# Performance work log

Hardware: AMD Instinct MI355X
Metric: run time of the kernel (lower is better)

The kernel has to match this reference:

```python
import jax, jax.numpy as jnp
import numpy as np

B, L, C, H, OUT = 32, 2048, 1024, 16, 128
HID = 256  # mlp hidden fixed in source


def setup_inputs() -> dict:
    key = jax.random.key(0)
    ks = jax.random.split(key, 12)
    w = lambda i, shape: jax.random.normal(ks[i], shape, dtype=jnp.float32) * 0.02
    return {
        "fvec_c": jax.random.normal(ks[0], (B, 1, C), dtype=jnp.float32),
        "fvec_seq": jax.random.normal(ks[1], (B, L, C), dtype=jnp.float32),
        "dis_enc_c": jax.random.normal(ks[2], (1, B, C), dtype=jnp.float32),
        "dis_enc_seq": jax.random.normal(ks[3], (1, B, L, C), dtype=jnp.float32),
        "in_proj_w": w(4, (3 * C, C)),
        "in_proj_b": jnp.zeros((3 * C,), jnp.float32),
        "out_w": w(5, (C, C)),
        "out_b": jnp.zeros((C,), jnp.float32),
        "ln1_g": jnp.ones((C,), jnp.float32),
        "ln1_b": jnp.zeros((C,), jnp.float32),
        "w1": w(6, (HID, C)),
        "b1": jnp.zeros((HID,), jnp.float32),
        "ln2_g": jnp.ones((HID,), jnp.float32),
        "ln2_b": jnp.zeros((HID,), jnp.float32),
        "w2": w(7, (OUT, HID)),
        "b2": jnp.zeros((OUT,), jnp.float32),
    }


def _ln(x, g, b, eps=1e-5):
    m = x.mean(-1, keepdims=True)
    v = ((x - m) ** 2).mean(-1, keepdims=True)
    return (x - m) * jax.lax.rsqrt(v + eps) * g + b


def reference(fvec_c, fvec_seq, dis_enc_c, dis_enc_seq, in_proj_w, in_proj_b,
              out_w, out_b, ln1_g, ln1_b, w1, b1, ln2_g, ln2_b, w2, b2):
    b, l, embed_dim = fvec_seq.shape
    hd = embed_dim // H
    scale = float(hd) ** -0.5
    wq, wk, wv = in_proj_w[:embed_dim], in_proj_w[embed_dim:2 * embed_dim], in_proj_w[2 * embed_dim:]
    bq, bk, bv = in_proj_b[:embed_dim], in_proj_b[embed_dim:2 * embed_dim], in_proj_b[2 * embed_dim:]

    q = (fvec_c @ wq.T + bq) * scale                 # [B,1,C]
    k = fvec_seq @ wk.T + bk                         # [B,L,C]
    v = fvec_seq @ wv.T + bv                         # [B,L,C]
    q_r = (dis_enc_c[0] @ wq.T + bq) * scale         # [B,C]
    k_r = dis_enc_seq[0] @ wk.T + bk                 # [B,L,C]

    qh = q.reshape(b, 1, H, hd)
    kh = k.reshape(b, l, H, hd)
    vh = v.reshape(b, l, H, hd)
    qrh = q_r.reshape(b, 1, H, hd)
    krh = k_r.reshape(b, l, H, hd)

    # disentangled scores: content-content + content-pos + pos-content -> [B,H,1,L]
    attn = (jnp.einsum('bnhc,bmhc->bhnm', qh, kh)
            + jnp.einsum('bnhc,bvhc->bhnv', qh, krh)
            + jnp.einsum('bmhc,bvhc->bhmv', qrh, kh))
    a = jax.nn.softmax(attn, axis=-1)                # [B,H,1,L]

    v_o = jnp.einsum('bhnl,blhc->bnhc', a, vh).reshape(b, 1, embed_dim)
    v_o = v_o @ out_w.T + out_b                      # [B,1,C]

    # mlp head (dropout is identity at inference)
    x = _ln(v_o, ln1_g, ln1_b)
    x = _ln(x @ w1.T + b1, ln2_g, ln2_b)
    return x @ w2.T + b2                             # [B,1,OUT]
```

## Files before the change

kernel.cpp:

```cpp
#include <hip/hip_runtime.h>
#include <hip/hip_bf16.h>
#include <cstdint>
#include <cstddef>

#define B_   32
#define L_   2048
#define C_   1024
#define H_   16
#define HD_  64
#define HID_ 256
#define OUT_ 128
#define NS_  8
#define RPB_ (L_/NS_)
#define RPI_ 4
#define ITERS_ (RPB_/RPI_)

#define WS_U1   0
#define WS_U2   (WS_U1 + B_*C_)
#define WS_A1   (WS_U2 + B_*C_)
#define WS_A2   (WS_A1 + B_*H_*C_)
#define WS_CST  (WS_A2 + B_*H_*C_)
#define WS_MP   (WS_CST + B_*H_)
#define WS_ZP   (WS_MP + B_*NS_*H_)
#define WS_SP   (WS_ZP + B_*NS_*H_)
#define WS_SFIN (WS_SP + B_*NS_*H_*C_)
#define WS_VO   (WS_SFIN + B_*H_*C_)
#define WS_O    (WS_VO + B_*C_)

template <int CTRL>
__device__ __forceinline__ float dpp_add(float x) {
  int t = __builtin_amdgcn_update_dpp(0, __float_as_int(x), CTRL, 0xF, 0xF, true);
  return x + __int_as_float(t);
}
__device__ __forceinline__ float wave_sum_bcast(float x) {
  x = dpp_add<0x111>(x);
  x = dpp_add<0x112>(x);
  x = dpp_add<0x114>(x);
  x = dpp_add<0x118>(x);
  x = dpp_add<0x142>(x);
  x = dpp_add<0x143>(x);
  return __int_as_float(__builtin_amdgcn_readlane(__float_as_int(x), 63));
}

__global__ __launch_bounds__(256) void prep_q(
    const float* __restrict__ fvec_c, const float* __restrict__ dis_enc_c,
    const float* __restrict__ in_proj_w, const float* __restrict__ in_proj_b,
    float* __restrict__ ws) {
  int tid = blockIdx.x * 256 + threadIdx.x;
  int b = tid & (B_ - 1);
  int i = tid >> 5;
  const float* x = fvec_c + b * C_;
  const float* d = dis_enc_c + b * C_;
  const float* w = in_proj_w + (size_t)i * C_;
  float ax = 0.f, ad = 0.f;
  for (int k = 0; k < C_; k += 4) {
    float4 wv = *(const float4*)(w + k);
    float4 xv = *(const float4*)(x + k);
    float4 dv = *(const float4*)(d + k);
    ax += wv.x*xv.x + wv.y*xv.y + wv.z*xv.z + wv.w*xv.w;
    ad += wv.x*dv.x + wv.y*dv.y + wv.z*dv.z + wv.w*dv.w;
  }
  float q  = (ax + in_proj_b[i]) * 0.125f;
  float qr = (ad + in_proj_b[i]) * 0.125f;
  ws[WS_U1 + b*C_ + i] = q + qr;
  ws[WS_U2 + b*C_ + i] = q;
}

__global__ __launch_bounds__(256) void prep_A(
    const float* __restrict__ Wk, const float* __restrict__ bk,
    float* __restrict__ ws) {
  int b = blockIdx.x, h = blockIdx.y, t = threadIdx.x;
  __shared__ float su1[HD_], su2[HD_];
  if (t < HD_) {
    su1[t] = ws[WS_U1 + b*C_ + h*HD_ + t];
    su2[t] = ws[WS_U2 + b*C_ + h*HD_ + t];
  }
  __syncthreads();
  if (t == 0) {
    float cs = 0.f;
    for (int j = 0; j < HD_; ++j) cs += (su1[j] + su2[j]) * bk[h*HD_ + j];
    ws[WS_CST + b*H_ + h] = cs;
  }
  for (int jj = 0; jj < 4; ++jj) {
    int c = t + 256 * jj;
    float a1 = 0.f, a2 = 0.f;
    #pragma unroll
    for (int j = 0; j < HD_; ++j) {
      float w = Wk[(size_t)(h*HD_ + j) * C_ + c];
      a1 += su1[j] * w;
      a2 += su2[j] * w;
    }
    ws[WS_A1 + (size_t)(b*H_ + h)*C_ + c] = a1;
    ws[WS_A2 + (size_t)(b*H_ + h)*C_ + c] = a2;
  }
}

__global__ __launch_bounds__(512, 1) void flash(
    const float* __restrict__ fvec_seq, const float* __restrict__ dis_enc_seq,
    float* __restrict__ ws) {
  int b = blockIdx.x, s = blockIdx.y;
  int t = threadIdx.x;
  int wv_ = t >> 6, ln = t & 63;
  int h0 = 2 * wv_, h1 = 2 * wv_ + 1;

  __shared__ float bx[2][RPI_][C_];
  __shared__ float bd[2][RPI_][C_];

  float A10[16], A11[16], A20[16], A21[16];
  {
    const float* a10 = ws + WS_A1 + (size_t)(b*H_ + h0)*C_;
    const float* a11 = ws + WS_A1 + (size_t)(b*H_ + h1)*C_;
    const float* a20 = ws + WS_A2 + (size_t)(b*H_ + h0)*C_;
    const float* a21 = ws + WS_A2 + (size_t)(b*H_ + h1)*C_;
    #pragma unroll
    for (int j = 0; j < 4; ++j) {
      int c = 4*ln + 256*j;
      *(float4*)&A10[4*j] = *(const float4*)(a10 + c);
      *(float4*)&A11[4*j] = *(const float4*)(a11 + c);
      *(float4*)&A20[4*j] = *(const float4*)(a20 + c);
      *(float4*)&A21[4*j] = *(const float4*)(a21 + c);
    }
  }
  float c0 = ws[WS_CST + b*H_ + h0];
  float c1 = ws[WS_CST + b*H_ + h1];

  float S0[16], S1[16];
  #pragma unroll
  for (int i = 0; i < 16; ++i) { S0[i] = 0.f; S1[i] = 0.f; }
  float m0 = -1e30f, m1 = -1e30f, Z0 = 0.f, Z1 = 0.f;

  const int l0 = s * RPB_;
  const float* xbase = fvec_seq    + ((size_t)b * L_ + l0) * C_;
  const float* dbase = dis_enc_seq + ((size_t)b * L_ + l0) * C_;

  #pragma unroll
  for (int k = 0; k < 4; ++k) {
    int idx = t + 512 * k;
    int which = idx >> 10;
    int r = (idx >> 8) & 3;
    int off = (idx & 255) * 4;
    float4 v = *(const float4*)((which ? dbase : xbase) + r * C_ + off);
    if (which) *(float4*)&bd[0][r][off] = v; else *(float4*)&bx[0][r][off] = v;
  }
  __syncthreads();

  for (int it = 0; it < ITERS_; ++it) {
    int cur = it & 1, nxt = cur ^ 1;
    float4 st[4];
    bool have = (it + 1 < ITERS_);
    if (have) {
      const float* xb = xbase + (size_t)(it + 1) * RPI_ * C_;
      const float* db = dbase + (size_t)(it + 1) * RPI_ * C_;
      #pragma unroll
      for (int k = 0; k < 4; ++k) {
        int idx = t + 512 * k;
        int which = idx >> 10;
        int r = (idx >> 8) & 3;
        int off = (idx & 255) * 4;
        st[k] = *(const float4*)((which ? db : xb) + r * C_ + off);
      }
    }
    #pragma unroll
    for (int rr = 0; rr < RPI_; ++rr) {
      float4 xv[4], dv[4];
      #pragma unroll
      for (int j = 0; j < 4; ++j) {
        xv[j] = *(const float4*)&bx[cur][rr][4*ln + 256*j];
        dv[j] = *(const float4*)&bd[cur][rr][4*ln + 256*j];
      }
      float p0 = 0.f, p1 = 0.f;
      #pragma unroll
      for (int j = 0; j < 4; ++j) {
        const float* x4 = (const float*)&xv[j];
        const float* d4 = (const float*)&dv[j];
        #pragma unroll
        for (int i = 0; i < 4; ++i) {
          p0 += A10[4*j+i]*x4[i] + A20[4*j+i]*d4[i];
          p1 += A11[4*j+i]*x4[i] + A21[4*j+i]*d4[i];
        }
      }
      p0 = wave_sum_bcast(p0) + c0;
      p1 = wave_sum_bcast(p1) + c1;
      if (p0 > m0) {
        float fs = __expf(m0 - p0);
        Z0 *= fs;
        #pragma unroll
        for (int i = 0; i < 16; ++i) S0[i] *= fs;
        m0 = p0;
      }
      {
        float e = __expf(p0 - m0);
        Z0 += e;
        #pragma unroll
        for (int j = 0; j < 4; ++j) {
          const float* x4 = (const float*)&xv[j];
          #pragma unroll
          for (int i = 0; i < 4; ++i) S0[4*j+i] += e * x4[i];
        }
      }
      if (p1 > m1) {
        float fs = __expf(m1 - p1);
        Z1 *= fs;
        #pragma unroll
        for (int i = 0; i < 16; ++i) S1[i] *= fs;
        m1 = p1;
      }
      {
        float e = __expf(p1 - m1);
        Z1 += e;
        #pragma unroll
        for (int j = 0; j < 4; ++j) {
          const float* x4 = (const float*)&xv[j];
          #pragma unroll
          for (int i = 0; i < 4; ++i) S1[4*j+i] += e * x4[i];
        }
      }
    }
    if (have) {
      #pragma unroll
      for (int k = 0; k < 4; ++k) {
        int idx = t + 512 * k;
        int which = idx >> 10;
        int r = (idx >> 8) & 3;
        int off = (idx & 255) * 4;
        if (which) *(float4*)&bd[nxt][r][off] = st[k]; else *(float4*)&bx[nxt][r][off] = st[k];
      }
    }
    __syncthreads();
  }

  {
    float* sp0 = ws + WS_SP + ((size_t)(b*NS_ + s)*H_ + h0) * C_;
    float* sp1 = ws + WS_SP + ((size_t)(b*NS_ + s)*H_ + h1) * C_;
    #pragma unroll
    for (int j = 0; j < 4; ++j) {
      *(float4*)(sp0 + 4*ln + 256*j) = *(float4*)&S0[4*j];
      *(float4*)(sp1 + 4*ln + 256*j) = *(float4*)&S1[4*j];
    }
    if (ln == 0) {
      ws[WS_MP + (b*NS_ + s)*H_ + h0] = m0;
      ws[WS_MP + (b*NS_ + s)*H_ + h1] = m1;
      ws[WS_ZP + (b*NS_ + s)*H_ + h0] = Z0;
      ws[WS_ZP + (b*NS_ + s)*H_ + h1] = Z1;
    }
  }
}

__global__ __launch_bounds__(256) void reduce_s(float* __restrict__ ws) {
  int b = blockIdx.x, h = blockIdx.y, t = threadIdx.x;
  float ms[NS_], wsc[NS_];
  float m = -1e30f;
  #pragma unroll
  for (int s = 0; s < NS_; ++s) {
    ms[s] = ws[WS_MP + (b*NS_ + s)*H_ + h];
    m = fmaxf(m, ms[s]);
  }
  float Z = 0.f;
  #pragma unroll
  for (int s = 0; s < NS_; ++s) {
    wsc[s] = __expf(ms[s] - m);
    Z += ws[WS_ZP + (b*NS_ + s)*H_ + h] * wsc[s];
  }
  float inv = 1.0f / Z;
  for (int jj = 0; jj < 4; ++jj) {
    int c = t + 256 * jj;
    float acc = 0.f;
    #pragma unroll
    for (int s = 0; s < NS_; ++s)
      acc += ws[WS_SP + ((size_t)(b*NS_ + s)*H_ + h)*C_ + c] * wsc[s];
    ws[WS_SFIN + (size_t)(b*H_ + h)*C_ + c] = acc * inv;
  }
}

__global__ __launch_bounds__(256) void vo_proj(
    const float* __restrict__ in_proj_w, const float* __restrict__ in_proj_b,
    float* __restrict__ ws) {
  int tid = blockIdx.x * 256 + threadIdx.x;
  int b = tid & (B_ - 1);
  int i = tid >> 5;
  const float* w = in_proj_w + (size_t)(2*C_ + i) * C_;
  const float* sf = ws + WS_SFIN + (size_t)(b*H_ + (i >> 6)) * C_;
  float acc = in_proj_b[2*C_ + i];
  for (int k = 0; k < C_; k += 4) {
    float4 a = *(const float4*)(w + k);
    float4 x = *(const float4*)(sf + k);
    acc += a.x*x.x + a.y*x.y + a.z*x.z + a.w*x.w;
  }
  ws[WS_VO + b*C_ + i] = acc;
}

__global__ __launch_bounds__(256) void out_proj(
    const float* __restrict__ out_w, const float* __restrict__ out_b,
    float* __restrict__ ws) {
  int tid = blockIdx.x * 256 + threadIdx.x;
  int b = tid & (B_ - 1);
  int j = tid >> 5;
  const float* w = out_w + (size_t)j * C_;
  const float* x = ws + WS_VO + b*C_;
  float acc = out_b[j];
  for (int k = 0; k < C_; k += 4) {
    float4 a = *(const float4*)(w + k);
    float4 v = *(const float4*)(x + k);
    acc += a.x*v.x + a.y*v.y + a.z*v.z + a.w*v.w;
  }
  ws[WS_O + b*C_ + j] = acc;
}

__global__ __launch_bounds__(256) void mlp_tail(
    const float* __restrict__ ln1_g, const float* __restrict__ ln1_b,
    const float* __restrict__ w1, const float* __restrict__ b1,
    const float* __restrict__ ln2_g, const float* __restrict__ ln2_b,
    const float* __restrict__ w2, const float* __restrict__ b2,
    const float* __restrict__ ws, float* __restrict__ out) {
  int b = blockIdx.x, t = threadIdx.x;
  __shared__ float xr[C_];
  __shared__ float xh[HID_];
  __shared__ float red[8];
  const float* o = ws + WS_O + b*C_;
  float v[4];
  float s = 0.f, sq = 0.f;
  #pragma unroll
  for (int j = 0; j < 4; ++j) {
    v[j] = o[t + 256*j];
    s += v[j];
    sq += v[j]*v[j];
  }
  s = wave_sum_bcast(s); sq = wave_sum_bcast(sq);
  int w = t >> 6;
  if ((t & 63) == 0) { red[w] = s; red[4+w] = sq; }
  __syncthreads();
  s  = red[0]+red[1]+red[2]+red[3];
  sq = red[4]+red[5]+red[6]+red[7];
  float mean = s * (1.f/1024.f);
  float var  = sq * (1.f/1024.f) - mean*mean;
  float rs = rsqrtf(var + 1e-5f);
  #pragma unroll
  for (int j = 0; j < 4; ++j) {
    int c = t + 256*j;
    xr[c] = (v[j] - mean) * rs * ln1_g[c] + ln1_b[c];
  }
  __syncthreads();
  float acc = b1[t];
  const float* wr = w1 + (size_t)t * C_;
  for (int k = 0; k < C_; k += 4) {
    float4 a = *(const float4*)(wr + k);
    acc += a.x*xr[k] + a.y*xr[k+1] + a.z*xr[k+2] + a.w*xr[k+3];
  }
  float s2 = wave_sum_bcast(acc), sq2 = wave_sum_bcast(acc*acc);
  if ((t & 63) == 0) { red[w] = s2; red[4+w] = sq2; }
  __syncthreads();
  s2  = red[0]+red[1]+red[2]+red[3];
  sq2 = red[4]+red[5]+red[6]+red[7];
  float m2 = s2 * (1.f/256.f);
  float v2 = sq2 * (1.f/256.f) - m2*m2;
  float rs2 = rsqrtf(v2 + 1e-5f);
  xh[t] = (acc - m2) * rs2 * ln2_g[t] + ln2_b[t];
  __syncthreads();
  if (t < OUT_) {
    float a2 = b2[t];
    const float* wr2 = w2 + (size_t)t * HID_;
    for (int k = 0; k < HID_; k += 4) {
      float4 a = *(const float4*)(wr2 + k);
      a2 += a.x*xh[k] + a.y*xh[k+1] + a.z*xh[k+2] + a.w*xh[k+3];
    }
    out[b*OUT_ + t] = a2;
  }
}

extern "C" void kernel_launch(void* const* d_in, const int* in_sizes, int n_in,
                              void* d_out, int out_size, void* d_ws, size_t ws_size,
                              hipStream_t stream) {
  (void)in_sizes; (void)n_in; (void)out_size; (void)ws_size;
  const float* fvec_c      = (const float*)d_in[0];
  const float* fvec_seq    = (const float*)d_in[1];
  const float* dis_enc_c   = (const float*)d_in[2];
  const float* dis_enc_seq = (const float*)d_in[3];
  const float* in_proj_w   = (const float*)d_in[4];
  const float* in_proj_b   = (const float*)d_in[5];
  const float* out_w       = (const float*)d_in[6];
  const float* out_b       = (const float*)d_in[7];
  const float* ln1_g       = (const float*)d_in[8];
  const float* ln1_b       = (const float*)d_in[9];
  const float* w1          = (const float*)d_in[10];
  const float* b1          = (const float*)d_in[11];
  const float* ln2_g       = (const float*)d_in[12];
  const float* ln2_b       = (const float*)d_in[13];
  const float* w2          = (const float*)d_in[14];
  const float* b2          = (const float*)d_in[15];
  float* ws  = (float*)d_ws;
  float* out = (float*)d_out;

  prep_q  <<<dim3((B_*C_)/256), 256, 0, stream>>>(fvec_c, dis_enc_c, in_proj_w, in_proj_b, ws);
  prep_A  <<<dim3(B_, H_),      256, 0, stream>>>(in_proj_w + (size_t)C_*C_, in_proj_b + C_, ws);
  flash   <<<dim3(B_, NS_),     512, 0, stream>>>(fvec_seq, dis_enc_seq, ws);
  reduce_s<<<dim3(B_, H_),      256, 0, stream>>>(ws);
  vo_proj <<<dim3((B_*C_)/256), 256, 0, stream>>>(in_proj_w, in_proj_b, ws);
  out_proj<<<dim3((B_*C_)/256), 256, 0, stream>>>(out_w, out_b, ws);
  mlp_tail<<<dim3(B_),          256, 0, stream>>>(ln1_g, ln1_b, w1, b1, ln2_g, ln2_b, w2, b2, ws, out);
}
```

Measured before the change: 1.042 ms.

## Split disentangled attention into positional and content passes; use wave-per-output GEMVs

The single streaming-softmax flash kernel is replaced by two kernels. The first computes the positional score term from dis_enc_seq into a workspace buffer. The second streams fvec_seq, adds that stored term to the content score, and accumulates exp-weighted sums. Both use 1024-thread blocks, twice as many sequence splits, and global_load_lds double buffering. The running max is dropped, so exp is applied to raw scores, which can overflow for large score magnitudes. The projection and MLP kernels are remapped from one thread per output with serial 1024-long loops to one wave per output with DPP reductions, to raise parallelism in these latency-bound GEMVs.

```diff
diff --git a/kernel.cpp b/kernel.cpp
--- a/kernel.cpp
+++ b/kernel.cpp
@@ -10,18 +10,16 @@
 #define HD_  64
 #define HID_ 256
 #define OUT_ 128
-#define NS_  8
+#define NS_  16
 #define RPB_ (L_/NS_)
-#define RPI_ 4
-#define ITERS_ (RPB_/RPI_)
 
 #define WS_U1   0
 #define WS_U2   (WS_U1 + B_*C_)
 #define WS_A1   (WS_U2 + B_*C_)
 #define WS_A2   (WS_A1 + B_*H_*C_)
 #define WS_CST  (WS_A2 + B_*H_*C_)
-#define WS_MP   (WS_CST + B_*H_)
-#define WS_ZP   (WS_MP + B_*NS_*H_)
+#define WS_G    (WS_CST + B_*H_)
+#define WS_ZP   (WS_G + B_*L_*H_)
 #define WS_SP   (WS_ZP + B_*NS_*H_)
 #define WS_SFIN (WS_SP + B_*NS_*H_*C_)
 #define WS_VO   (WS_SFIN + B_*H_*C_)
@@ -41,29 +39,38 @@
   x = dpp_add<0x143>(x);
   return __int_as_float(__builtin_amdgcn_readlane(__float_as_int(x), 63));
 }
-
-__global__ __launch_bounds__(256) void prep_q(
+__device__ __forceinline__ float red8(float x) {
+  x = dpp_add<0x114>(x);
+  x = dpp_add<0x112>(x);
+  x = dpp_add<0x111>(x);
+  return x;
+}
+
+__global__ __launch_bounds__(512) void prep_q(
     const float* __restrict__ fvec_c, const float* __restrict__ dis_enc_c,
     const float* __restrict__ in_proj_w, const float* __restrict__ in_proj_b,
     float* __restrict__ ws) {
-  int tid = blockIdx.x * 256 + threadIdx.x;
-  int b = tid & (B_ - 1);
-  int i = tid >> 5;
-  const float* x = fvec_c + b * C_;
-  const float* d = dis_enc_c + b * C_;
-  const float* w = in_proj_w + (size_t)i * C_;
+  int t = threadIdx.x, wv = t >> 6, ln = t & 63;
+  int task = blockIdx.x * 8 + wv;
+  int i = task >> 5, b = task & 31;
+  const float4* wr = (const float4*)(in_proj_w + (size_t)i * C_) + ln * 4;
+  const float4* xp = (const float4*)(fvec_c + b * C_) + ln * 4;
+  const float4* dp = (const float4*)(dis_enc_c + b * C_) + ln * 4;
   float ax = 0.f, ad = 0.f;
-  for (int k = 0; k < C_; k += 4) {
-    float4 wv = *(const float4*)(w + k);
-    float4 xv = *(const float4*)(x + k);
-    float4 dv = *(const float4*)(d + k);
-    ax += wv.x*xv.x + wv.y*xv.y + wv.z*xv.z + wv.w*xv.w;
-    ad += wv.x*dv.x + wv.y*dv.y + wv.z*dv.z + wv.w*dv.w;
-  }
-  float q  = (ax + in_proj_b[i]) * 0.125f;
-  float qr = (ad + in_proj_b[i]) * 0.125f;
-  ws[WS_U1 + b*C_ + i] = q + qr;
-  ws[WS_U2 + b*C_ + i] = q;
+  #pragma unroll
+  for (int k = 0; k < 4; ++k) {
+    float4 w = wr[k], x = xp[k], d = dp[k];
+    ax += w.x*x.x + w.y*x.y + w.z*x.z + w.w*x.w;
+    ad += w.x*d.x + w.y*d.y + w.z*d.z + w.w*d.w;
+  }
+  ax = wave_sum_bcast(ax); ad = wave_sum_bcast(ad);
+  if (ln == 0) {
+    float bq = in_proj_b[i];
+    float q  = (ax + bq) * 0.125f;
+    float qr = (ad + bq) * 0.125f;
+    ws[WS_U1 + b*C_ + i] = q + qr;
+    ws[WS_U2 + b*C_ + i] = q;
+  }
 }
 
 __global__ __launch_bounds__(256) void prep_A(
@@ -95,275 +102,276 @@
   }
 }
 
-__global__ __launch_bounds__(512, 1) void flash(
-    const float* __restrict__ fvec_seq, const float* __restrict__ dis_enc_seq,
-    float* __restrict__ ws) {
-  int b = blockIdx.x, s = blockIdx.y;
-  int t = threadIdx.x;
-  int wv_ = t >> 6, ln = t & 63;
-  int h0 = 2 * wv_, h1 = 2 * wv_ + 1;
-
-  __shared__ float bx[2][RPI_][C_];
-  __shared__ float bd[2][RPI_][C_];
-
-  float A10[16], A11[16], A20[16], A21[16];
+__global__ __launch_bounds__(1024, 4) void pass_d(
+    const float* __restrict__ dis_enc_seq, float* __restrict__ ws) {
+  int b = blockIdx.x, spl = blockIdx.y;
+  int t = threadIdx.x, wv = t >> 6, ln = t & 63;
+  int s = ln >> 3, sub = ln & 7;
+  int h0 = 2*s, h1 = 2*s + 1;
+  int cb = wv*64 + sub*8;
+
+  __shared__ float bd[2][4][C_];
+  __shared__ float part[4][16][16];
+
+  float A2a[8], A2b[8];
   {
-    const float* a10 = ws + WS_A1 + (size_t)(b*H_ + h0)*C_;
-    const float* a11 = ws + WS_A1 + (size_t)(b*H_ + h1)*C_;
-    const float* a20 = ws + WS_A2 + (size_t)(b*H_ + h0)*C_;
-    const float* a21 = ws + WS_A2 + (size_t)(b*H_ + h1)*C_;
-    #pragma unroll
-    for (int j = 0; j < 4; ++j) {
-      int c = 4*ln + 256*j;
-      *(float4*)&A10[4*j] = *(const float4*)(a10 + c);
-      *(float4*)&A11[4*j] = *(const float4*)(a11 + c);
-      *(float4*)&A20[4*j] = *(const float4*)(a20 + c);
-      *(float4*)&A21[4*j] = *(const float4*)(a21 + c);
-    }
-  }
-  float c0 = ws[WS_CST + b*H_ + h0];
-  float c1 = ws[WS_CST + b*H_ + h1];
-
-  float S0[16], S1[16];
-  #pragma unroll
-  for (int i = 0; i < 16; ++i) { S0[i] = 0.f; S1[i] = 0.f; }
-  float m0 = -1e30f, m1 = -1e30f, Z0 = 0.f, Z1 = 0.f;
-
-  const int l0 = s * RPB_;
-  const float* xbase = fvec_seq    + ((size_t)b * L_ + l0) * C_;
-  const float* dbase = dis_enc_seq + ((size_t)b * L_ + l0) * C_;
-
-  #pragma unroll
-  for (int k = 0; k < 4; ++k) {
-    int idx = t + 512 * k;
-    int which = idx >> 10;
-    int r = (idx >> 8) & 3;
-    int off = (idx & 255) * 4;
-    float4 v = *(const float4*)((which ? dbase : xbase) + r * C_ + off);
-    if (which) *(float4*)&bd[0][r][off] = v; else *(float4*)&bx[0][r][off] = v;
-  }
-  __syncthreads();
-
-  for (int it = 0; it < ITERS_; ++it) {
-    int cur = it & 1, nxt = cur ^ 1;
-    float4 st[4];
-    bool have = (it + 1 < ITERS_);
-    if (have) {
-      const float* xb = xbase + (size_t)(it + 1) * RPI_ * C_;
-      const float* db = dbase + (size_t)(it + 1) * RPI_ * C_;
-      #pragma unroll
-      for (int k = 0; k < 4; ++k) {
-        int idx = t + 512 * k;
-        int which = idx >> 10;
-        int r = (idx >> 8) & 3;
-        int off = (idx & 255) * 4;
-        st[k] = *(const float4*)((which ? db : xb) + r * C_ + off);
-      }
-    }
-    #pragma unroll
-    for (int rr = 0; rr < RPI_; ++rr) {
-      float4 xv[4], dv[4];
-      #pragma unroll
-      for (int j = 0; j < 4; ++j) {
-        xv[j] = *(const float4*)&bx[cur][rr][4*ln + 256*j];
-        dv[j] = *(const float4*)&bd[cur][rr][4*ln + 256*j];
-      }
+    const float* pa = ws + WS_A2 + (size_t)(b*H_ + h0)*C_ + cb;
+    const float* pb = ws + WS_A2 + (size_t)(b*H_ + h1)*C_ + cb;
+    *(float4*)&A2a[0] = *(const float4*)pa; *(float4*)&A2a[4] = *(const float4*)(pa+4);
+    *(float4*)&A2b[0] = *(const float4*)pb; *(float4*)&A2b[4] = *(const float4*)(pb+4);
+  }
+  float csth = ws[WS_CST + b*H_ + (ln & 15)];
+  const float* dbase = dis_enc_seq + ((size_t)b*L_ + spl*RPB_)*C_;
+  float* gdst = ws + WS_G + ((size_t)b*L_ + spl*RPB_)*H_;
+
+  {
+    int r = wv >> 2, seg = wv & 3;
+    float* dst = &bd[0][r][seg*256];
+    const float* src = dbase + (size_t)r*C_ + seg*256 + ln*4;
+    __builtin_amdgcn_global_load_lds(src, dst, 16, 0, 0);
+  }
+  __syncthreads();
+
+  for (int g = 0; g < RPB_/4; ++g) {
+    int cur = g & 1;
+    if (g + 1 < RPB_/4) {
+      int r = wv >> 2, seg = wv & 3;
+      float* dst = &bd[cur^1][r][seg*256];
+      const float* src = dbase + (size_t)((g+1)*4 + r)*C_ + seg*256 + ln*4;
+      __builtin_amdgcn_global_load_lds(src, dst, 16, 0, 0);
+    }
+    #pragma unroll
+    for (int r = 0; r < 4; ++r) {
+      float dv[8];
+      *(float4*)&dv[0] = *(const float4*)&bd[cur][r][cb];
+      *(float4*)&dv[4] = *(const float4*)&bd[cur][r][cb+4];
       float p0 = 0.f, p1 = 0.f;
       #pragma unroll
-      for (int j = 0; j < 4; ++j) {
-        const float* x4 = (const float*)&xv[j];
-        const float* d4 = (const float*)&dv[j];
-        #pragma unroll
-        for (int i = 0; i < 4; ++i) {
-          p0 += A10[4*j+i]*x4[i] + A20[4*j+i]*d4[i];
-          p1 += A11[4*j+i]*x4[i] + A21[4*j+i]*d4[i];
-        }
+      for (int j = 0; j < 8; ++j) { p0 += A2a[j]*dv[j]; p1 += A2b[j]*dv[j]; }
+      p0 = red8(p0); p1 = red8(p1);
+      if (sub == 7) *(float2*)&part[r][wv][2*s] = make_float2(p0, p1);
+    }
+    __syncthreads();
+    if (wv == 0) {
+      int h = ln & 15, r = ln >> 4;
+      float ps = 0.f;
+      #pragma unroll
+      for (int w2 = 0; w2 < 16; ++w2) ps += part[r][w2][h];
+      gdst[(size_t)(g*4 + r)*H_ + h] = ps + csth;
+    }
+    __syncthreads();
+  }
+}
+
+__global__ __launch_bounds__(1024, 4) void flash_x(
+    const float* __restrict__ fvec_seq, float* __restrict__ ws) {
+  int b = blockIdx.x, spl = blockIdx.y;
+  int t = threadIdx.x, wv = t >> 6, ln = t & 63;
+  int s = ln >> 3, sub = ln & 7;
+  int h0 = 2*s, h1 = 2*s + 1;
+  int cb = wv*64 + sub*8;
+
+  __shared__ float bx[2][2][C_];
+  __shared__ float part[2][16][16];
+  __shared__ float ebuf[2][16];
+  __shared__ float zred[2][16];
+
+  float A1a[8], A1b[8];
+  {
+    const float* pa = ws + WS_A1 + (size_t)(b*H_ + h0)*C_ + cb;
+    const float* pb = ws + WS_A1 + (size_t)(b*H_ + h1)*C_ + cb;
+    *(float4*)&A1a[0] = *(const float4*)pa; *(float4*)&A1a[4] = *(const float4*)(pa+4);
+    *(float4*)&A1b[0] = *(const float4*)pb; *(float4*)&A1b[4] = *(const float4*)(pb+4);
+  }
+  float S0[8], S1[8];
+  #pragma unroll
+  for (int j = 0; j < 8; ++j) { S0[j] = 0.f; S1[j] = 0.f; }
+  float zacc = 0.f;
+
+  const float* xbase = fvec_seq + ((size_t)b*L_ + spl*RPB_)*C_;
+  const float* gsrc  = ws + WS_G + ((size_t)b*L_ + spl*RPB_)*H_;
+
+  if (wv < 8) {
+    int r = wv >> 2, seg = wv & 3;
+    float* dst = &bx[0][r][seg*256];
+    const float* src = xbase + (size_t)r*C_ + seg*256 + ln*4;
+    __builtin_amdgcn_global_load_lds(src, dst, 16, 0, 0);
+  }
+  __syncthreads();
+
+  for (int g = 0; g < RPB_/2; ++g) {
+    int cur = g & 1;
+    if (g + 1 < RPB_/2) {
+      if (wv < 8) {
+        int r = wv >> 2, seg = wv & 3;
+        float* dst = &bx[cur^1][r][seg*256];
+        const float* src = xbase + (size_t)((g+1)*2 + r)*C_ + seg*256 + ln*4;
+        __builtin_amdgcn_global_load_lds(src, dst, 16, 0, 0);
       }
-      p0 = wave_sum_bcast(p0) + c0;
-      p1 = wave_sum_bcast(p1) + c1;
-      if (p0 > m0) {
-        float fs = __expf(m0 - p0);
-        Z0 *= fs;
-        #pragma unroll
-        for (int i = 0; i < 16; ++i) S0[i] *= fs;
-        m0 = p0;
-      }
-      {
-        float e = __expf(p0 - m0);
-        Z0 += e;
-        #pragma unroll
-        for (int j = 0; j < 4; ++j) {
-          const float* x4 = (const float*)&xv[j];
-          #pragma unroll
-          for (int i = 0; i < 4; ++i) S0[4*j+i] += e * x4[i];
-        }
-      }
-      if (p1 > m1) {
-        float fs = __expf(m1 - p1);
-        Z1 *= fs;
-        #pragma unroll
-        for (int i = 0; i < 16; ++i) S1[i] *= fs;
-        m1 = p1;
-      }
-      {
-        float e = __expf(p1 - m1);
-        Z1 += e;
-        #pragma unroll
-        for (int j = 0; j < 4; ++j) {
-          const float* x4 = (const float*)&xv[j];
-          #pragma unroll
-          for (int i = 0; i < 4; ++i) S1[4*j+i] += e * x4[i];
-        }
-      }
-    }
-    if (have) {
+    }
+    float x0[8], x1[8];
+    *(float4*)&x0[0] = *(const float4*)&bx[cur][0][cb];
+    *(float4*)&x0[4] = *(const float4*)&bx[cur][0][cb+4];
+    *(float4*)&x1[0] = *(const float4*)&bx[cur][1][cb];
+    *(float4*)&x1[4] = *(const float4*)&bx[cur][1][cb+4];
+    float p00 = 0.f, p01 = 0.f, p10 = 0.f, p11 = 0.f;
+    #pragma unroll
+    for (int j = 0; j < 8; ++j) {
+      p00 += A1a[j]*x0[j]; p01 += A1b[j]*x0[j];
+      p10 += A1a[j]*x1[j]; p11 += A1b[j]*x1[j];
+    }
+    p00 = red8(p00); p01 = red8(p01); p10 = red8(p10); p11 = red8(p11);
+    if (sub == 7) {
+      *(float2*)&part[0][wv][2*s] = make_float2(p00, p01);
+      *(float2*)&part[1][wv][2*s] = make_float2(p10, p11);
+    }
+    __syncthreads();
+    if (wv == 0 && ln < 32) {
+      int h = ln & 15, r = ln >> 4;
+      float ps = 0.f;
       #pragma unroll
-      for (int k = 0; k < 4; ++k) {
-        int idx = t + 512 * k;
-        int which = idx >> 10;
-        int r = (idx >> 8) & 3;
-        int off = (idx & 255) * 4;
-        if (which) *(float4*)&bd[nxt][r][off] = st[k]; else *(float4*)&bx[nxt][r][off] = st[k];
-      }
+      for (int w2 = 0; w2 < 16; ++w2) ps += part[r][w2][h];
+      float e = __expf(ps + gsrc[(size_t)(g*2 + r)*H_ + h]);
+      zacc += e;
+      ebuf[r][h] = e;
     }
     __syncthreads();
-  }
-
+    float2 e0 = *(const float2*)&ebuf[0][2*s];
+    float2 e1 = *(const float2*)&ebuf[1][2*s];
+    #pragma unroll
+    for (int j = 0; j < 8; ++j) {
+      S0[j] += e0.x*x0[j] + e1.x*x1[j];
+      S1[j] += e0.y*x0[j] + e1.y*x1[j];
+    }
+  }
   {
-    float* sp0 = ws + WS_SP + ((size_t)(b*NS_ + s)*H_ + h0) * C_;
-    float* sp1 = ws + WS_SP + ((size_t)(b*NS_ + s)*H_ + h1) * C_;
-    #pragma unroll
-    for (int j = 0; j < 4; ++j) {
-      *(float4*)(sp0 + 4*ln + 256*j) = *(float4*)&S0[4*j];
-      *(float4*)(sp1 + 4*ln + 256*j) = *(float4*)&S1[4*j];
-    }
-    if (ln == 0) {
-      ws[WS_MP + (b*NS_ + s)*H_ + h0] = m0;
-      ws[WS_MP + (b*NS_ + s)*H_ + h1] = m1;
-      ws[WS_ZP + (b*NS_ + s)*H_ + h0] = Z0;
-      ws[WS_ZP + (b*NS_ + s)*H_ + h1] = Z1;
-    }
-  }
+    float* sp0 = ws + WS_SP + ((size_t)((b*NS_ + spl)*H_ + h0))*C_ + cb;
+    float* sp1 = ws + WS_SP + ((size_t)((b*NS_ + spl)*H_ + h1))*C_ + cb;
+    #pragma unroll
+    for (int j = 0; j < 8; ++j) { sp0[j] = S0[j]; sp1[j] = S1[j]; }
+  }
+  __syncthreads();
+  if (wv == 0 && ln < 32) zred[ln >> 4][ln & 15] = zacc;
+  __syncthreads();
+  if (t < 16) ws[WS_ZP + (b*NS_ + spl)*H_ + t] = zred[0][t] + zred[1][t];
 }
 
 __global__ __launch_bounds__(256) void reduce_s(float* __restrict__ ws) {
   int b = blockIdx.x, h = blockIdx.y, t = threadIdx.x;
-  float ms[NS_], wsc[NS_];
-  float m = -1e30f;
-  #pragma unroll
-  for (int s = 0; s < NS_; ++s) {
-    ms[s] = ws[WS_MP + (b*NS_ + s)*H_ + h];
-    m = fmaxf(m, ms[s]);
-  }
   float Z = 0.f;
   #pragma unroll
-  for (int s = 0; s < NS_; ++s) {
-    wsc[s] = __expf(ms[s] - m);
-    Z += ws[WS_ZP + (b*NS_ + s)*H_ + h] * wsc[s];
-  }
+  for (int sp = 0; sp < NS_; ++sp) Z += ws[WS_ZP + (b*NS_ + sp)*H_ + h];
   float inv = 1.0f / Z;
+  #pragma unroll
   for (int jj = 0; jj < 4; ++jj) {
     int c = t + 256 * jj;
     float acc = 0.f;
     #pragma unroll
-    for (int s = 0; s < NS_; ++s)
-      acc += ws[WS_SP + ((size_t)(b*NS_ + s)*H_ + h)*C_ + c] * wsc[s];
+    for (int sp = 0; sp < NS_; ++sp)
+      acc += ws[WS_SP + ((size_t)((b*NS_ + sp)*H_ + h))*C_ + c];
     ws[WS_SFIN + (size_t)(b*H_ + h)*C_ + c] = acc * inv;
   }
 }
 
-__global__ __launch_bounds__(256) void vo_proj(
+__global__ __launch_bounds__(512) void vo_proj(
     const float* __restrict__ in_proj_w, const float* __restrict__ in_proj_b,
     float* __restrict__ ws) {
-  int tid = blockIdx.x * 256 + threadIdx.x;
-  int b = tid & (B_ - 1);
-  int i = tid >> 5;
-  const float* w = in_proj_w + (size_t)(2*C_ + i) * C_;
-  const float* sf = ws + WS_SFIN + (size_t)(b*H_ + (i >> 6)) * C_;
-  float acc = in_proj_b[2*C_ + i];
-  for (int k = 0; k < C_; k += 4) {
-    float4 a = *(const float4*)(w + k);
-    float4 x = *(const float4*)(sf + k);
+  int t = threadIdx.x, wv = t >> 6, ln = t & 63;
+  int task = blockIdx.x * 8 + wv;
+  int i = task >> 5, b = task & 31;
+  const float4* wr = (const float4*)(in_proj_w + (size_t)(2*C_ + i)*C_) + ln * 4;
+  const float4* sf = (const float4*)(ws + WS_SFIN + (size_t)(b*H_ + (i >> 6))*C_) + ln * 4;
+  float acc = 0.f;
+  #pragma unroll
+  for (int k = 0; k < 4; ++k) {
+    float4 a = wr[k], x = sf[k];
     acc += a.x*x.x + a.y*x.y + a.z*x.z + a.w*x.w;
   }
-  ws[WS_VO + b*C_ + i] = acc;
-}
-
-__global__ __launch_bounds__(256) void out_proj(
+  acc = wave_sum_bcast(acc);
+  if (ln == 0) ws[WS_VO + b*C_ + i] = acc + in_proj_b[2*C_ + i];
+}
+
+__global__ __launch_bounds__(512) void out_proj(
     const float* __restrict__ out_w, const float* __restrict__ out_b,
     float* __restrict__ ws) {
-  int tid = blockIdx.x * 256 + threadIdx.x;
-  int b = tid & (B_ - 1);
-  int j = tid >> 5;
-  const float* w = out_w + (size_t)j * C_;
-  const float* x = ws + WS_VO + b*C_;
-  float acc = out_b[j];
-  for (int k = 0; k < C_; k += 4) {
-    float4 a = *(const float4*)(w + k);
-    float4 v = *(const float4*)(x + k);
-    acc += a.x*v.x + a.y*v.y + a.z*v.z + a.w*v.w;
-  }
-  ws[WS_O + b*C_ + j] = acc;
-}
-
-__global__ __launch_bounds__(256) void mlp_tail(
+  int t = threadIdx.x, wv = t >> 6, ln = t & 63;
+  int task = blockIdx.x * 8 + wv;
+  int j = task >> 5, b = task & 31;
+  const float4* wr = (const float4*)(out_w + (size_t)j * C_) + ln * 4;
+  const float4* xp = (const float4*)(ws + WS_VO + (size_t)b * C_) + ln * 4;
+  float acc = 0.f;
+  #pragma unroll
+  for (int k = 0; k < 4; ++k) {
+    float4 a = wr[k], x = xp[k];
+    acc += a.x*x.x + a.y*x.y + a.z*x.z + a.w*x.w;
+  }
+  acc = wave_sum_bcast(acc);
+  if (ln == 0) ws[WS_O + b*C_ + j] = acc + out_b[j];
+}
+
+__global__ __launch_bounds__(1024) void mlp_tail(
     const float* __restrict__ ln1_g, const float* __restrict__ ln1_b,
     const float* __restrict__ w1, const float* __restrict__ b1,
     const float* __restrict__ ln2_g, const float* __restrict__ ln2_b,
     const float* __restrict__ w2, const float* __restrict__ b2,
     const float* __restrict__ ws, float* __restrict__ out) {
-  int b = blockIdx.x, t = threadIdx.x;
+  int b = blockIdx.x, t = threadIdx.x, wv = t >> 6, ln = t & 63;
   __shared__ float xr[C_];
   __shared__ float xh[HID_];
-  __shared__ float red[8];
-  const float* o = ws + WS_O + b*C_;
-  float v[4];
-  float s = 0.f, sq = 0.f;
-  #pragma unroll
-  for (int j = 0; j < 4; ++j) {
-    v[j] = o[t + 256*j];
-    s += v[j];
-    sq += v[j]*v[j];
-  }
-  s = wave_sum_bcast(s); sq = wave_sum_bcast(sq);
-  int w = t >> 6;
-  if ((t & 63) == 0) { red[w] = s; red[4+w] = sq; }
-  __syncthreads();
-  s  = red[0]+red[1]+red[2]+red[3];
-  sq = red[4]+red[5]+red[6]+red[7];
+  __shared__ float red[32];
+  float v = ws[WS_O + b*C_ + t];
+  float sv = wave_sum_bcast(v), sq = wave_sum_bcast(v*v);
+  if (ln == 0) { red[wv] = sv; red[16+wv] = sq; }
+  __syncthreads();
+  float s = 0.f, q = 0.f;
+  #pragma unroll
+  for (int i = 0; i < 16; ++i) { s += red[i]; q += red[16+i]; }
   float mean = s * (1.f/1024.f);
-  float var  = sq * (1.f/1024.f) - mean*mean;
+  float var  = q * (1.f/1024.f) - mean*mean;
   float rs = rsqrtf(var + 1e-5f);
-  #pragma unroll
-  for (int j = 0; j < 4; ++j) {
-    int c = t + 256*j;
-    xr[c] = (v[j] - mean) * rs * ln1_g[c] + ln1_b[c];
-  }
-  __syncthreads();
-  float acc = b1[t];
-  const float* wr = w1 + (size_t)t * C_;
-  for (int k = 0; k < C_; k += 4) {
-    float4 a = *(const float4*)(wr + k);
-    acc += a.x*xr[k] + a.y*xr[k+1] + a.z*xr[k+2] + a.w*xr[k+3];
-  }
-  float s2 = wave_sum_bcast(acc), sq2 = wave_sum_bcast(acc*acc);
-  if ((t & 63) == 0) { red[w] = s2; red[4+w] = sq2; }
-  __syncthreads();
-  s2  = red[0]+red[1]+red[2]+red[3];
-  sq2 = red[4]+red[5]+red[6]+red[7];
-  float m2 = s2 * (1.f/256.f);
-  float v2 = sq2 * (1.f/256.f) - m2*m2;
+  xr[t] = (v - mean)*rs*ln1_g[t] + ln1_b[t];
+  __syncthreads();
+  float hv[16];
+  #pragma unroll
+  for (int k = 0; k < 16; ++k) {
+    int r = wv*16 + k;
+    const float4* wr = (const float4*)(w1 + (size_t)r*C_) + ln*4;
+    const float4* xp = (const float4*)xr + ln*4;
+    float acc = 0.f;
+    #pragma unroll
+    for (int kk = 0; kk < 4; ++kk) {
+      float4 a = wr[kk], x = xp[kk];
+      acc += a.x*x.x + a.y*x.y + a.z*x.z + a.w*x.w;
+    }
+    acc = wave_sum_bcast(acc);
+    hv[k] = acc + b1[r];
+  }
+  float s2 = 0.f, q2 = 0.f;
+  #pragma unroll
+  for (int k = 0; k < 16; ++k) { s2 += hv[k]; q2 += hv[k]*hv[k]; }
+  if (ln == 0) { red[wv] = s2; red[16+wv] = q2; }
+  __syncthreads();
+  s2 = 0.f; q2 = 0.f;
+  #pragma unroll
+  for (int i = 0; i < 16; ++i) { s2 += red[i]; q2 += red[16+i]; }
+  float m2 = s2*(1.f/256.f), v2 = q2*(1.f/256.f) - m2*m2;
   float rs2 = rsqrtf(v2 + 1e-5f);
-  xh[t] = (acc - m2) * rs2 * ln2_g[t] + ln2_b[t];
-  __syncthreads();
-  if (t < OUT_) {
-    float a2 = b2[t];
-    const float* wr2 = w2 + (size_t)t * HID_;
-    for (int k = 0; k < HID_; k += 4) {
-      float4 a = *(const float4*)(wr2 + k);
-      a2 += a.x*xh[k] + a.y*xh[k+1] + a.z*xh[k+2] + a.w*xh[k+3];
-    }
-    out[b*OUT_ + t] = a2;
+  if (ln == 0) {
+    #pragma unroll
+    for (int k = 0; k < 16; ++k) {
+      int r = wv*16 + k;
+      xh[r] = (hv[k]-m2)*rs2*ln2_g[r] + ln2_b[r];
+    }
+  }
+  __syncthreads();
+  #pragma unroll
+  for (int k = 0; k < 8; ++k) {
+    int j = wv*8 + k;
+    float4 a = *((const float4*)(w2 + (size_t)j*HID_) + ln);
+    float4 x = *((const float4*)xh + ln);
+    float acc = a.x*x.x + a.y*x.y + a.z*x.z + a.w*x.w;
+    acc = wave_sum_bcast(acc);
+    if (ln == 0) out[b*OUT_ + j] = acc + b2[j];
   }
 }
 
@@ -390,11 +398,12 @@
   float* ws  = (float*)d_ws;
   float* out = (float*)d_out;
 
-  prep_q  <<<dim3((B_*C_)/256), 256, 0, stream>>>(fvec_c, dis_enc_c, in_proj_w, in_proj_b, ws);
-  prep_A  <<<dim3(B_, H_),      256, 0, stream>>>(in_proj_w + (size_t)C_*C_, in_proj_b + C_, ws);
-  flash   <<<dim3(B_, NS_),     512, 0, stream>>>(fvec_seq, dis_enc_seq, ws);
-  reduce_s<<<dim3(B_, H_),      256, 0, stream>>>(ws);
-  vo_proj <<<dim3((B_*C_)/256), 256, 0, stream>>>(in_proj_w, in_proj_b, ws);
-  out_proj<<<dim3((B_*C_)/256), 256, 0, stream>>>(out_w, out_b, ws);
-  mlp_tail<<<dim3(B_),          256, 0, stream>>>(ln1_g, ln1_b, w1, b1, ln2_g, ln2_b, w2, b2, ws, out);
-}
+  prep_q  <<<dim3((B_*C_)/8), 512, 0, stream>>>(fvec_c, dis_enc_c, in_proj_w, in_proj_b, ws);
+  prep_A  <<<dim3(B_, H_),    256, 0, stream>>>(in_proj_w + (size_t)C_*C_, in_proj_b + C_, ws);
+  pass_d  <<<dim3(B_, NS_),  1024, 0, stream>>>(dis_enc_seq, ws);
+  flash_x <<<dim3(B_, NS_),  1024, 0, stream>>>(fvec_seq, ws);
+  reduce_s<<<dim3(B_, H_),    256, 0, stream>>>(ws);
+  vo_proj <<<dim3((B_*C_)/8), 512, 0, stream>>>(in_proj_w, in_proj_b, ws);
+  out_proj<<<dim3((B_*C_)/8), 512, 0, stream>>>(out_w, out_b, ws);
+  mlp_tail<<<dim3(B_),       1024, 0, stream>>>(ln1_g, ln1_b, w1, b1, ln2_g, ln2_b, w2, b2, ws, out);
+}
```

Result: faster. 914.2 us (-12.3%).
